# Optimization experiments

Hardware: AMD Instinct MI355X
Metric: run time of the kernel (lower is better)

## Reference

```python
import jax, jax.numpy as jnp
import numpy as np

B, T, F, H, L = 16384, 24, 7, 8, 4
DENSE = [T * H, 1024, 2048, 4]


def setup_inputs() -> dict:
    key = jax.random.key(0)
    d = {"x": jax.random.normal(jax.random.fold_in(key, 0), (B, T, F), jnp.float32)}
    k = 1
    s = 1.0 / np.sqrt(H)  # torch LSTM init bound
    for l in range(L):
        in_dim = F if l == 0 else H
        for name, shape in [("Wih", (4 * H, in_dim)), ("Whh", (4 * H, H)), ("bih", (4 * H,)), ("bhh", (4 * H,))]:
            d[f"{name}{l}"] = jax.random.uniform(jax.random.fold_in(key, k), shape, jnp.float32, -s, s)
            k += 1
    for i in range(1, len(DENSE)):
        si = 1.0 / np.sqrt(DENSE[i - 1])
        d[f"Wd{i}"] = jax.random.uniform(jax.random.fold_in(key, k), (DENSE[i], DENSE[i - 1]), jnp.float32, -si, si)
        k += 1
        d[f"bd{i}"] = jax.random.uniform(jax.random.fold_in(key, k), (DENSE[i],), jnp.float32, -si, si)
        k += 1
    return d


def _lstm_layer(xs, Wih, Whh, b):
    # xs: [T, B, in] -> ys: [T, B, H]; torch gate order i,f,g,o
    Hn = Whh.shape[1]
    h0 = jnp.zeros((xs.shape[1], Hn), xs.dtype)

    def step(carry, xt):
        h, c = carry
        z = xt @ Wih.T + h @ Whh.T + b  # [B, 4H]
        i, f, g, o = jnp.split(z, 4, axis=-1)
        c = jax.nn.sigmoid(f) * c + jax.nn.sigmoid(i) * jnp.tanh(g)
        h = jax.nn.sigmoid(o) * jnp.tanh(c)
        return (h, c), h

    (_, _), ys = jax.lax.scan(step, (h0, h0), xs)
    return ys


def _forward(x, lstm_params, dense_params):
    xs = jnp.transpose(x, (1, 0, 2))  # [T, B, F]
    for (Wih, Whh, bih, bhh) in lstm_params:
        xs = _lstm_layer(xs, Wih, Whh, bih + bhh)
    out = jnp.transpose(xs, (1, 0, 2)).reshape(x.shape[0], T * H)  # [B, 192]
    (W1, b1), (W2, b2), (W3, b3) = dense_params
    out = jax.nn.relu(out @ W1.T + b1)
    out = jax.nn.relu(out @ W2.T + b2)
    return out @ W3.T + b3  # [B, num_classes]


def reference(x, Wih0, Whh0, bih0, bhh0, Wih1, Whh1, bih1, bhh1, Wih2, Whh2, bih2, bhh2, Wih3, Whh3, bih3, bhh3, Wd1, bd1, Wd2, bd2, Wd3, bd3):
    lstm_params = [(Wih0, Whh0, bih0, bhh0), (Wih1, Whh1, bih1, bhh1), (Wih2, Whh2, bih2, bhh2), (Wih3, Whh3, bih3, bhh3)]
    dense_params = [(Wd1, bd1), (Wd2, bd2), (Wd3, bd3)]
    return _forward(x, lstm_params, dense_params)
```

## Files before the change

kernel.cpp:

```cpp
#include <hip/hip_runtime.h>
#include <hip/hip_bf16.h>

typedef __attribute__((ext_vector_type(4))) float f32x4;
typedef __attribute__((ext_vector_type(8))) short bf16x8;

__device__ __forceinline__ ushort f2bf(float f) {
    union { float f; uint u; } v; v.f = f;
    uint u = v.u;
    return (ushort)((u + 0x7fffu + ((u >> 16) & 1u)) >> 16);
}
__device__ __forceinline__ float bf2f(ushort h) {
    union { uint u; float f; } v; v.u = ((uint)h) << 16;
    return v.f;
}
__device__ __forceinline__ float sigm(float x) {
    return __builtin_amdgcn_rcpf(1.0f + __builtin_amdgcn_exp2f(x * -1.442695040888963f));
}
__device__ __forceinline__ float tanh_(float x) {
    return 2.0f * __builtin_amdgcn_rcpf(1.0f + __builtin_amdgcn_exp2f(x * -2.885390081777927f)) - 1.0f;
}

typedef const __attribute__((address_space(1))) unsigned int ga_u32;
typedef __attribute__((address_space(3))) unsigned int lds_u32;
__device__ __forceinline__ void g2l16(const void* g, void* l) {
    __builtin_amdgcn_global_load_lds((ga_u32*)(unsigned long long)g,
                                     (lds_u32*)(unsigned int)(unsigned long long)l,
                                     16, 0, 0);
}

struct LstmW {
    const float* wih[4];
    const float* whh[4];
    const float* bih[4];
    const float* bhh[4];
};

__device__ __forceinline__ void gates8(const float wx[4][8], const float xv8[8],
                                       float& a0, float& a1, float& a2, float& a3) {
#pragma unroll
    for (int k = 0; k < 8; ++k) {
        float xv = xv8[k];
        a0 += wx[0][k] * xv; a1 += wx[1][k] * xv;
        a2 += wx[2][k] * xv; a3 += wx[3][k] * xv;
    }
}
__device__ __forceinline__ void cellup(float a0, float a1, float a2, float a3,
                                       float& h, float& c) {
    c = sigm(a1) * c + sigm(a0) * tanh_(a2);
    h = sigm(a3) * tanh_(c);
}
__device__ __forceinline__ void ld8(const float* p, float v[8]) {
    float4 a = *(const float4*)p;
    float4 b = *(const float4*)(p + 4);
    v[0] = a.x; v[1] = a.y; v[2] = a.z; v[3] = a.w;
    v[4] = b.x; v[5] = b.y; v[6] = b.z; v[7] = b.w;
}

__global__ __launch_bounds__(256) void pre_kernel(const float* __restrict__ x, LstmW p,
                                                  ushort* __restrict__ Y,
                                                  const float* __restrict__ W1,
                                                  const float* __restrict__ W2,
                                                  ushort* __restrict__ W1b,
                                                  ushort* __restrict__ W2b,
                                                  const float* __restrict__ b3,
                                                  float* __restrict__ out) {
    __shared__ float xs[32 * 168];
    __shared__ float hb[32 * 200];

    const int tid = threadIdx.x;
    if (blockIdx.x >= 512) {
        const int tg = (blockIdx.x - 512) * 256 + tid;
        if (tg < 16384) {
            float4 bv = {b3[0], b3[1], b3[2], b3[3]};
            ((float4*)out)[tg] = bv;
        }
#pragma unroll
        for (int s = 0; s < 4; ++s) {
            int i = tg + s * 143360;
            const float4* src; ushort4* dst; int off;
            if (i < 49152) { src = (const float4*)W1; dst = (ushort4*)W1b; off = i; }
            else { src = (const float4*)W2; dst = (ushort4*)W2b; off = i - 49152; }
            float4 v = src[off];
            ushort4 r; r.x = f2bf(v.x); r.y = f2bf(v.y); r.z = f2bf(v.z); r.w = f2bf(v.w);
            dst[off] = r;
        }
        return;
    }

    const int e0 = blockIdx.x * 32;
    {
        const float4* s = (const float4*)(x + (size_t)e0 * 168);
        float4* d = (float4*)xs;
        for (int i = tid; i < 1344; i += 256) d[i] = s[i];
    }
    __syncthreads();

    const int el = tid >> 3, j = tid & 7;
    float* hr = hb + el * 200;
    const float* xr = xs + el * 168;

    float wx[4][8], wh[4][8], bs4[4];

    {
        const float* Wih = p.wih[0];
        const float* Whh = p.whh[0];
#pragma unroll
        for (int g = 0; g < 4; ++g) {
#pragma unroll
            for (int k = 0; k < 7; ++k) wx[g][k] = Wih[(g * 8 + j) * 7 + k];
#pragma unroll
            for (int k = 0; k < 8; ++k) wh[g][k] = Whh[(g * 8 + j) * 8 + k];
            bs4[g] = p.bih[0][g * 8 + j] + p.bhh[0][g * 8 + j];
        }
        float h = 0.f, c = 0.f;
        {
            float a0 = bs4[0], a1 = bs4[1], a2 = bs4[2], a3 = bs4[3];
#pragma unroll
            for (int k = 0; k < 7; ++k) {
                float xv = xr[k];
                a0 += wx[0][k] * xv; a1 += wx[1][k] * xv;
                a2 += wx[2][k] * xv; a3 += wx[3][k] * xv;
            }
            cellup(a0, a1, a2, a3, h, c);
            hr[j] = h;
        }
        for (int t = 1; t < 24; ++t) {
            float a0 = bs4[0], a1 = bs4[1], a2 = bs4[2], a3 = bs4[3];
#pragma unroll
            for (int k = 0; k < 7; ++k) {
                float xv = xr[t * 7 + k];
                a0 += wx[0][k] * xv; a1 += wx[1][k] * xv;
                a2 += wx[2][k] * xv; a3 += wx[3][k] * xv;
            }
            float hp[8]; ld8(&hr[(t - 1) * 8], hp);
            gates8(wh, hp, a0, a1, a2, a3);
            cellup(a0, a1, a2, a3, h, c);
            hr[t * 8 + j] = h;
        }
    }

#pragma unroll
    for (int l = 1; l < 4; ++l) {
        const float* Wih = p.wih[l];
        const float* Whh = p.whh[l];
#pragma unroll
        for (int g = 0; g < 4; ++g) {
#pragma unroll
            for (int k = 0; k < 8; ++k) {
                wx[g][k] = Wih[(g * 8 + j) * 8 + k];
                wh[g][k] = Whh[(g * 8 + j) * 8 + k];
            }
            bs4[g] = p.bih[l][g * 8 + j] + p.bhh[l][g * 8 + j];
        }
        float h = 0.f, c = 0.f;
        {
            float xin[8]; ld8(&hr[0], xin);
            float a0 = bs4[0], a1 = bs4[1], a2 = bs4[2], a3 = bs4[3];
            gates8(wx, xin, a0, a1, a2, a3);
            cellup(a0, a1, a2, a3, h, c);
            hr[j] = h;
            if (l == 3) Y[((size_t)(e0 + el) * 24) * 8 + j] = f2bf(h);
        }
        for (int t = 1; t < 24; ++t) {
            float xin[8]; ld8(&hr[t * 8], xin);
            float hp[8];  ld8(&hr[(t - 1) * 8], hp);
            float a0 = bs4[0], a1 = bs4[1], a2 = bs4[2], a3 = bs4[3];
            gates8(wx, xin, a0, a1, a2, a3);
            gates8(wh, hp, a0, a1, a2, a3);
            cellup(a0, a1, a2, a3, h, c);
            hr[t * 8 + j] = h;
            if (l == 3) Y[((size_t)(e0 + el) * 24 + t) * 8 + j] = f2bf(h);
        }
    }
}

template <int KDIM, bool FUSE3>
__global__ __launch_bounds__(256) void gemm_kernel(const ushort* __restrict__ A,
                                                   const ushort* __restrict__ W,
                                                   const float* __restrict__ bias,
                                                   ushort* __restrict__ Hout,
                                                   const float* __restrict__ W3,
                                                   float* __restrict__ outf, int N) {
    constexpr int SMEMN = FUSE3 ? 17408 : 16384;
    __shared__ ushort smem[SMEMN];
    __shared__ float w3s[FUSE3 ? 512 : 1];
    ushort* As = smem;
    ushort* Ws = smem + 8192;

    const int tid = threadIdx.x;
    const int m0 = blockIdx.x * 128;
    const int n0 = blockIdx.y * 128;
    const int lane = tid & 63;
    const int wv = tid >> 6;
    const int wm = (wv & 1) * 64;
    const int wn = (wv >> 1) * 64;
    const int m16 = lane & 15;
    const int quad = lane >> 4;

    if (FUSE3) {
        for (int i = tid; i < 512; i += 256)
            w3s[i] = W3[(size_t)(i >> 7) * 2048 + n0 + (i & 127)];
    }

    f32x4 acc[4][4];
    const f32x4 zero = {0.f, 0.f, 0.f, 0.f};
#pragma unroll
    for (int mi = 0; mi < 4; ++mi)
#pragma unroll
        for (int ni = 0; ni < 4; ++ni) acc[mi][ni] = zero;

    const int lrow = lane >> 3;
    const int lchunk = (lane & 7) ^ lrow;
    const ushort* Ag = A + (size_t)(m0 + wv * 32 + lrow) * KDIM + lchunk * 8;
    const ushort* Wg = W + (size_t)(n0 + wv * 32 + lrow) * KDIM + lchunk * 8;
    ushort* Ald = As + wv * 2048;
    ushort* Wld = Ws + wv * 2048;

    const int r7 = m16 & 7;
    const int ck0 = (quad ^ r7) * 8;
    const int ck1 = ((quad + 4) ^ r7) * 8;

    for (int k0 = 0; k0 < KDIM; k0 += 64) {
#pragma unroll
        for (int c = 0; c < 4; ++c)
            g2l16(Ag + (size_t)c * 8 * KDIM + k0, Ald + c * 512);
#pragma unroll
        for (int c = 0; c < 4; ++c)
            g2l16(Wg + (size_t)c * 8 * KDIM + k0, Wld + c * 512);
        __syncthreads();

#pragma unroll
        for (int kk = 0; kk < 2; ++kk) {
            const int ck = kk ? ck1 : ck0;
            bf16x8 bfr[4];
#pragma unroll
            for (int ni = 0; ni < 4; ++ni)
                bfr[ni] = *(const bf16x8*)&Ws[(wn + ni * 16 + m16) * 64 + ck];
#pragma unroll
            for (int mi = 0; mi < 4; ++mi) {
                bf16x8 afr = *(const bf16x8*)&As[(wm + mi * 16 + m16) * 64 + ck];
#pragma unroll
                for (int ni = 0; ni < 4; ++ni)
                    acc[mi][ni] = __builtin_amdgcn_mfma_f32_16x16x32_bf16(afr, bfr[ni],
                                                                         acc[mi][ni], 0, 0, 0);
            }
        }
        __syncthreads();
    }

    if (!FUSE3) {
#pragma unroll
        for (int ni = 0; ni < 4; ++ni) {
            const int col = n0 + wn + ni * 16 + m16;
            const float b = bias[col];
#pragma unroll
            for (int mi = 0; mi < 4; ++mi)
#pragma unroll
                for (int r = 0; r < 4; ++r) {
                    const int row = m0 + wm + mi * 16 + quad * 4 + r;
                    Hout[(size_t)row * N + col] = f2bf(fmaxf(acc[mi][ni][r] + b, 0.f));
                }
        }
    } else {
        ushort* Cs = smem;
#pragma unroll
        for (int ni = 0; ni < 4; ++ni) {
            const int cl = wn + ni * 16 + m16;
            const float b = bias[n0 + cl];
#pragma unroll
            for (int mi = 0; mi < 4; ++mi)
#pragma unroll
                for (int r = 0; r < 4; ++r) {
                    const int rl = wm + mi * 16 + quad * 4 + r;
                    Cs[rl * 136 + cl] = f2bf(fmaxf(acc[mi][ni][r] + b, 0.f));
                }
        }
        __syncthreads();
        const int r = tid & 127;
        const int na = tid >> 7;
        const ushort* crow = &Cs[r * 136];
        float p0 = 0.f, p1 = 0.f;
#pragma unroll
        for (int ch = 0; ch < 16; ++ch) {
            bf16x8 v = *(const bf16x8*)(crow + ch * 8);
#pragma unroll
            for (int q = 0; q < 8; ++q) {
                float f = bf2f((ushort)v[q]);
                p0 += f * w3s[na * 128 + ch * 8 + q];
                p1 += f * w3s[(na + 2) * 128 + ch * 8 + q];
            }
        }
        atomicAdd(&outf[(size_t)(m0 + r) * 4 + na], p0);
        atomicAdd(&outf[(size_t)(m0 + r) * 4 + na + 2], p1);
    }
}

extern "C" void kernel_launch(void* const* d_in, const int* in_sizes, int n_in,
                              void* d_out, int out_size, void* d_ws, size_t ws_size,
                              hipStream_t stream) {
    const float* x = (const float*)d_in[0];
    LstmW w;
    for (int l = 0; l < 4; ++l) {
        w.wih[l] = (const float*)d_in[1 + 4 * l];
        w.whh[l] = (const float*)d_in[2 + 4 * l];
        w.bih[l] = (const float*)d_in[3 + 4 * l];
        w.bhh[l] = (const float*)d_in[4 + 4 * l];
    }
    const float* Wd1 = (const float*)d_in[17];
    const float* bd1 = (const float*)d_in[18];
    const float* Wd2 = (const float*)d_in[19];
    const float* bd2 = (const float*)d_in[20];
    const float* Wd3 = (const float*)d_in[21];
    const float* bd3 = (const float*)d_in[22];
    float* out = (float*)d_out;

    ushort* Y   = (ushort*)d_ws;
    ushort* H1  = (ushort*)((char*)d_ws + 6291456);
    ushort* W1b = (ushort*)((char*)d_ws + 39845888);
    ushort* W2b = (ushort*)((char*)d_ws + 40239104);

    pre_kernel<<<1072, 256, 0, stream>>>(x, w, Y, Wd1, Wd2, W1b, W2b, bd3, out);
    gemm_kernel<192, false><<<dim3(128, 8), 256, 0, stream>>>(Y, W1b, bd1, H1, nullptr, nullptr, 1024);
    gemm_kernel<1024, true><<<dim3(128, 16), 256, 0, stream>>>(H1, W2b, bd2, nullptr, Wd3, out, 2048);
}
```

Before: 245.1 us.

## Pack LSTM gate math into float2, swap GEMM grid order, fp32 fused W3 epilogue

The LSTM gate accumulation is repacked into float2 vectors so the compiler can emit packed FMA (v_pk_fma_f32) instructions. The GEMM grid is transposed so consecutive blocks share the same M tile of A, which is meant to improve L2 reuse of activations. The fused W3 epilogue now keeps the tile in fp32 in two half passes and uses vectorized LDS dot products instead of bf16 round-trips. The epilogue adds extra barriers and changes rounding slightly.

```diff
diff --git a/kernel.cpp b/kernel.cpp
--- a/kernel.cpp
+++ b/kernel.cpp
@@ -2,16 +2,13 @@
 #include <hip/hip_bf16.h>
 
 typedef __attribute__((ext_vector_type(4))) float f32x4;
+typedef __attribute__((ext_vector_type(2))) float f32x2;
 typedef __attribute__((ext_vector_type(8))) short bf16x8;
 
 __device__ __forceinline__ ushort f2bf(float f) {
     union { float f; uint u; } v; v.f = f;
     uint u = v.u;
     return (ushort)((u + 0x7fffu + ((u >> 16) & 1u)) >> 16);
-}
-__device__ __forceinline__ float bf2f(ushort h) {
-    union { uint u; float f; } v; v.u = ((uint)h) << 16;
-    return v.f;
 }
 __device__ __forceinline__ float sigm(float x) {
     return __builtin_amdgcn_rcpf(1.0f + __builtin_amdgcn_exp2f(x * -1.442695040888963f));
@@ -35,19 +32,18 @@
     const float* bhh[4];
 };
 
-__device__ __forceinline__ void gates8(const float wx[4][8], const float xv8[8],
-                                       float& a0, float& a1, float& a2, float& a3) {
+__device__ __forceinline__ void gates8p(const f32x2 w01[8], const f32x2 w23[8],
+                                        const float xv8[8], f32x2& a01, f32x2& a23) {
 #pragma unroll
     for (int k = 0; k < 8; ++k) {
-        float xv = xv8[k];
-        a0 += wx[0][k] * xv; a1 += wx[1][k] * xv;
-        a2 += wx[2][k] * xv; a3 += wx[3][k] * xv;
-    }
-}
-__device__ __forceinline__ void cellup(float a0, float a1, float a2, float a3,
-                                       float& h, float& c) {
-    c = sigm(a1) * c + sigm(a0) * tanh_(a2);
-    h = sigm(a3) * tanh_(c);
+        f32x2 xv = {xv8[k], xv8[k]};
+        a01 += w01[k] * xv;
+        a23 += w23[k] * xv;
+    }
+}
+__device__ __forceinline__ void cellup(f32x2 a01, f32x2 a23, float& h, float& c) {
+    c = sigm(a01.y) * c + sigm(a01.x) * tanh_(a23.x);
+    h = sigm(a23.y) * tanh_(c);
 }
 __device__ __forceinline__ void ld8(const float* p, float v[8]) {
     float4 a = *(const float4*)p;
@@ -99,42 +95,45 @@
     float* hr = hb + el * 200;
     const float* xr = xs + el * 168;
 
-    float wx[4][8], wh[4][8], bs4[4];
+    f32x2 wx01[8], wx23[8], wh01[8], wh23[8], b01, b23;
 
     {
         const float* Wih = p.wih[0];
         const float* Whh = p.whh[0];
 #pragma unroll
-        for (int g = 0; g < 4; ++g) {
-#pragma unroll
-            for (int k = 0; k < 7; ++k) wx[g][k] = Wih[(g * 8 + j) * 7 + k];
-#pragma unroll
-            for (int k = 0; k < 8; ++k) wh[g][k] = Whh[(g * 8 + j) * 8 + k];
-            bs4[g] = p.bih[0][g * 8 + j] + p.bhh[0][g * 8 + j];
-        }
+        for (int k = 0; k < 7; ++k) {
+            wx01[k] = {Wih[(0 + j) * 7 + k], Wih[(8 + j) * 7 + k]};
+            wx23[k] = {Wih[(16 + j) * 7 + k], Wih[(24 + j) * 7 + k]};
+        }
+#pragma unroll
+        for (int k = 0; k < 8; ++k) {
+            wh01[k] = {Whh[(0 + j) * 8 + k], Whh[(8 + j) * 8 + k]};
+            wh23[k] = {Whh[(16 + j) * 8 + k], Whh[(24 + j) * 8 + k]};
+        }
+        b01 = {p.bih[0][j] + p.bhh[0][j], p.bih[0][8 + j] + p.bhh[0][8 + j]};
+        b23 = {p.bih[0][16 + j] + p.bhh[0][16 + j], p.bih[0][24 + j] + p.bhh[0][24 + j]};
+
         float h = 0.f, c = 0.f;
         {
-            float a0 = bs4[0], a1 = bs4[1], a2 = bs4[2], a3 = bs4[3];
+            f32x2 a01 = b01, a23 = b23;
 #pragma unroll
             for (int k = 0; k < 7; ++k) {
-                float xv = xr[k];
-                a0 += wx[0][k] * xv; a1 += wx[1][k] * xv;
-                a2 += wx[2][k] * xv; a3 += wx[3][k] * xv;
-            }
-            cellup(a0, a1, a2, a3, h, c);
+                f32x2 xv = {xr[k], xr[k]};
+                a01 += wx01[k] * xv; a23 += wx23[k] * xv;
+            }
+            cellup(a01, a23, h, c);
             hr[j] = h;
         }
         for (int t = 1; t < 24; ++t) {
-            float a0 = bs4[0], a1 = bs4[1], a2 = bs4[2], a3 = bs4[3];
+            f32x2 a01 = b01, a23 = b23;
 #pragma unroll
             for (int k = 0; k < 7; ++k) {
-                float xv = xr[t * 7 + k];
-                a0 += wx[0][k] * xv; a1 += wx[1][k] * xv;
-                a2 += wx[2][k] * xv; a3 += wx[3][k] * xv;
+                f32x2 xv = {xr[t * 7 + k], xr[t * 7 + k]};
+                a01 += wx01[k] * xv; a23 += wx23[k] * xv;
             }
             float hp[8]; ld8(&hr[(t - 1) * 8], hp);
-            gates8(wh, hp, a0, a1, a2, a3);
-            cellup(a0, a1, a2, a3, h, c);
+            gates8p(wh01, wh23, hp, a01, a23);
+            cellup(a01, a23, h, c);
             hr[t * 8 + j] = h;
         }
     }
@@ -144,30 +143,31 @@
         const float* Wih = p.wih[l];
         const float* Whh = p.whh[l];
 #pragma unroll
-        for (int g = 0; g < 4; ++g) {
-#pragma unroll
-            for (int k = 0; k < 8; ++k) {
-                wx[g][k] = Wih[(g * 8 + j) * 8 + k];
-                wh[g][k] = Whh[(g * 8 + j) * 8 + k];
-            }
-            bs4[g] = p.bih[l][g * 8 + j] + p.bhh[l][g * 8 + j];
-        }
+        for (int k = 0; k < 8; ++k) {
+            wx01[k] = {Wih[(0 + j) * 8 + k], Wih[(8 + j) * 8 + k]};
+            wx23[k] = {Wih[(16 + j) * 8 + k], Wih[(24 + j) * 8 + k]};
+            wh01[k] = {Whh[(0 + j) * 8 + k], Whh[(8 + j) * 8 + k]};
+            wh23[k] = {Whh[(16 + j) * 8 + k], Whh[(24 + j) * 8 + k]};
+        }
+        b01 = {p.bih[l][j] + p.bhh[l][j], p.bih[l][8 + j] + p.bhh[l][8 + j]};
+        b23 = {p.bih[l][16 + j] + p.bhh[l][16 + j], p.bih[l][24 + j] + p.bhh[l][24 + j]};
+
         float h = 0.f, c = 0.f;
         {
             float xin[8]; ld8(&hr[0], xin);
-            float a0 = bs4[0], a1 = bs4[1], a2 = bs4[2], a3 = bs4[3];
-            gates8(wx, xin, a0, a1, a2, a3);
-            cellup(a0, a1, a2, a3, h, c);
+            f32x2 a01 = b01, a23 = b23;
+            gates8p(wx01, wx23, xin, a01, a23);
+            cellup(a01, a23, h, c);
             hr[j] = h;
             if (l == 3) Y[((size_t)(e0 + el) * 24) * 8 + j] = f2bf(h);
         }
         for (int t = 1; t < 24; ++t) {
             float xin[8]; ld8(&hr[t * 8], xin);
             float hp[8];  ld8(&hr[(t - 1) * 8], hp);
-            float a0 = bs4[0], a1 = bs4[1], a2 = bs4[2], a3 = bs4[3];
-            gates8(wx, xin, a0, a1, a2, a3);
-            gates8(wh, hp, a0, a1, a2, a3);
-            cellup(a0, a1, a2, a3, h, c);
+            f32x2 a01 = b01, a23 = b23;
+            gates8p(wx01, wx23, xin, a01, a23);
+            gates8p(wh01, wh23, hp, a01, a23);
+            cellup(a01, a23, h, c);
             hr[t * 8 + j] = h;
             if (l == 3) Y[((size_t)(e0 + el) * 24 + t) * 8 + j] = f2bf(h);
         }
@@ -182,14 +182,14 @@
                                                    const float* __restrict__ W3,
                                                    float* __restrict__ outf, int N) {
     constexpr int SMEMN = FUSE3 ? 17408 : 16384;
-    __shared__ ushort smem[SMEMN];
-    __shared__ float w3s[FUSE3 ? 512 : 1];
+    __shared__ alignas(16) ushort smem[SMEMN];
+    __shared__ alignas(16) float w3s[FUSE3 ? 528 : 1];
     ushort* As = smem;
     ushort* Ws = smem + 8192;
 
     const int tid = threadIdx.x;
-    const int m0 = blockIdx.x * 128;
-    const int n0 = blockIdx.y * 128;
+    const int n0 = blockIdx.x * 128;
+    const int m0 = blockIdx.y * 128;
     const int lane = tid & 63;
     const int wv = tid >> 6;
     const int wm = (wv & 1) * 64;
@@ -199,7 +199,7 @@
 
     if (FUSE3) {
         for (int i = tid; i < 512; i += 256)
-            w3s[i] = W3[(size_t)(i >> 7) * 2048 + n0 + (i & 127)];
+            w3s[(i >> 7) * 132 + (i & 127)] = W3[(size_t)(i >> 7) * 2048 + n0 + (i & 127)];
     }
 
     f32x4 acc[4][4];
@@ -262,36 +262,38 @@
                 }
         }
     } else {
-        ushort* Cs = smem;
-#pragma unroll
-        for (int ni = 0; ni < 4; ++ni) {
-            const int cl = wn + ni * 16 + m16;
-            const float b = bias[n0 + cl];
-#pragma unroll
-            for (int mi = 0; mi < 4; ++mi)
-#pragma unroll
-                for (int r = 0; r < 4; ++r) {
-                    const int rl = wm + mi * 16 + quad * 4 + r;
-                    Cs[rl * 136 + cl] = f2bf(fmaxf(acc[mi][ni][r] + b, 0.f));
+        float* Cs = (float*)smem;
+        const int drow = tid >> 2;
+        const int dn = tid & 3;
+#pragma unroll
+        for (int pass = 0; pass < 2; ++pass) {
+            if ((wv & 1) == pass) {
+#pragma unroll
+                for (int ni = 0; ni < 4; ++ni) {
+                    const int cl = wn + ni * 16 + m16;
+                    const float b = bias[n0 + cl];
+#pragma unroll
+                    for (int mi = 0; mi < 4; ++mi)
+#pragma unroll
+                        for (int r = 0; r < 4; ++r) {
+                            const int rl = mi * 16 + quad * 4 + r;
+                            Cs[rl * 132 + cl] = fmaxf(acc[mi][ni][r] + b, 0.f);
+                        }
                 }
-        }
-        __syncthreads();
-        const int r = tid & 127;
-        const int na = tid >> 7;
-        const ushort* crow = &Cs[r * 136];
-        float p0 = 0.f, p1 = 0.f;
-#pragma unroll
-        for (int ch = 0; ch < 16; ++ch) {
-            bf16x8 v = *(const bf16x8*)(crow + ch * 8);
-#pragma unroll
-            for (int q = 0; q < 8; ++q) {
-                float f = bf2f((ushort)v[q]);
-                p0 += f * w3s[na * 128 + ch * 8 + q];
-                p1 += f * w3s[(na + 2) * 128 + ch * 8 + q];
-            }
-        }
-        atomicAdd(&outf[(size_t)(m0 + r) * 4 + na], p0);
-        atomicAdd(&outf[(size_t)(m0 + r) * 4 + na + 2], p1);
+            }
+            __syncthreads();
+            const float* crow = &Cs[drow * 132];
+            const float* wrow = &w3s[dn * 132];
+            float p = 0.f;
+#pragma unroll
+            for (int ch = 0; ch < 32; ++ch) {
+                f32x4 cv = *(const f32x4*)(crow + ch * 4);
+                f32x4 wv4 = *(const f32x4*)(wrow + ch * 4);
+                p += cv[0] * wv4[0] + cv[1] * wv4[1] + cv[2] * wv4[2] + cv[3] * wv4[3];
+            }
+            atomicAdd(&outf[(size_t)(m0 + pass * 64 + drow) * 4 + dn], p);
+            __syncthreads();
+        }
     }
 }
 
@@ -320,6 +322,6 @@
     ushort* W2b = (ushort*)((char*)d_ws + 40239104);
 
     pre_kernel<<<1072, 256, 0, stream>>>(x, w, Y, Wd1, Wd2, W1b, W2b, bd3, out);
-    gemm_kernel<192, false><<<dim3(128, 8), 256, 0, stream>>>(Y, W1b, bd1, H1, nullptr, nullptr, 1024);
-    gemm_kernel<1024, true><<<dim3(128, 16), 256, 0, stream>>>(H1, W2b, bd2, nullptr, Wd3, out, 2048);
-}
+    gemm_kernel<192, false><<<dim3(8, 128), 256, 0, stream>>>(Y, W1b, bd1, H1, nullptr, nullptr, 1024);
+    gemm_kernel<1024, true><<<dim3(16, 128), 256, 0, stream>>>(H1, W2b, bd2, nullptr, Wd3, out, 2048);
+}
```

Result: faster. 235.0 us (-4.1%).
